# Optimization experiments

Measured on AMD Instinct MI355X. Metric: run time of the kernel, lower is better.

Reference implementation:

```python
import jax, jax.numpy as jnp
import numpy as np

K = 22                       # structuring element is 22x22 ones
ORIGIN = K // 2              # kornia origin = k//2 -> pad (11 before, 10 after)
PAD = ((0, 0), (0, 0), (ORIGIN, K - ORIGIN - 1), (ORIGIN, K - ORIGIN - 1))
WIN = (1, 1, K, K)
STRIDES = (1, 1, 1, 1)


def _erode(x):
    # flat (all-ones) structuring element erosion == sliding-window min.
    # Padding with +inf matches kornia's 'pad with max_val' for erosion.
    return jax.lax.reduce_window(x, float('inf'), jax.lax.min, WIN, STRIDES, PAD)


def _dilate(x):
    # flat dilation == sliding-window max; pad with -inf (kornia pads -max_val).
    return jax.lax.reduce_window(x, float('-inf'), jax.lax.max, WIN, STRIDES, PAD)


def setup_inputs() -> dict:
    key = jax.random.key(0)
    image = jax.random.uniform(key, (8, 3, 1024, 1024), dtype=jnp.float32)
    return {"image": image}


def reference(image):
    # morphological opening = erosion followed by dilation (same kernel)
    return _dilate(_erode(image))
```

## Files before the change

kernel.cpp:

```cpp
#include <hip/hip_runtime.h>


#define HH 1024
#define WW 1024
#define KW 22
#define SB 116
#define PINF __builtin_inff()

template<bool IS_MIN>
__device__ __forceinline__ float vop(float a, float b) {
    return IS_MIN ? fminf(a, b) : fmaxf(a, b);
}

template<bool IS_MIN, int COUT, class Get, class Put>
__device__ __forceinline__ void vanherk(Get get, Put put) {
    constexpr int NIN = COUT + KW - 1;
    constexpr int NB = (NIN + KW - 1) / KW;
    const float ID = IS_MIN ? PINF : -PINF;
    float Sprev[KW];
    #pragma unroll
    for (int j = 0; j < NB; ++j) {
        const int base = KW * j;
        const int needed = (NIN - base) < KW ? (NIN - base) : KW;
        float v[KW];
        #pragma unroll
        for (int m = 0; m < KW; ++m)
            if (m < needed) v[m] = get(base + m);
        float p = ID;
        #pragma unroll
        for (int m = 0; m < KW; ++m) {
            if (m < needed) {
                p = vop<IS_MIN>(p, v[m]);
                const int k = base - (KW - 1) + m;
                if (k >= 0 && k < COUT) {
                    if (m == KW - 1) put(k, p);
                    else             put(k, vop<IS_MIN>(Sprev[m + 1], p));
                }
            }
        }
        if (j < NB - 1) {
            float s = ID;
            #pragma unroll
            for (int m = KW - 1; m >= 0; --m) {
                s = vop<IS_MIN>(s, v[m]);
                Sprev[m] = s;
            }
        }
    }
}

template<bool INTERIOR>
__device__ __forceinline__ void tile_body(const float* __restrict__ src,
                                          float* __restrict__ dst,
                                          int R, int C, float* B, int t) {
    const int w = t >> 6, slot = t & 63;

    if (slot < 54) {
        const int ch = w >> 1;
        const int j = (w & 1) * 54 + slot;
        const int base_o = ch * 43;
        int cj = C - 22 + j;
        bool colOK = true;
        if (!INTERIOR) {
            colOK = (unsigned)cj < WW;
            cj = cj < 0 ? 0 : (cj > WW - 1 ? WW - 1 : cj);
        }
        const float* col = src + cj;
        const int rbase = R - 22 + base_o;
        vanherk<true, 43>(
            [&](int p) {
                int r = rbase + p;
                if (INTERIOR) return col[r * WW];
                int rc = r < 0 ? 0 : (r > HH - 1 ? HH - 1 : r);
                float vv = col[rc * WW];
                return (colOK && (unsigned)r < HH) ? vv : PINF;
            },
            [&](int k, float vv) { B[(base_o + k) * SB + j] = vv; });
    }
    __syncthreads();

    {
        const bool act = t < 255;
        const int ch = (3 * t + 2) >> 8;
        const int o = t - 85 * ch;
        const int g0 = 5 * ch;
        const int c0 = 20 * ch;
        float* Brow = B + o * SB;
        float in12[68];
        if (act) {
            #pragma unroll
            for (int i = 0; i < 17; ++i) {
                float4 x = ((const float4*)Brow)[g0 + i];
                in12[4 * i] = x.x; in12[4 * i + 1] = x.y;
                in12[4 * i + 2] = x.z; in12[4 * i + 3] = x.w;
            }
        }
        float rx[24];
        if (act) {
            float er[45];
            vanherk<true, 45>(
                [&](int p) { return in12[p]; },
                [&](int k, float vv) { er[k] = vv; });
            if (!INTERIOR) {
                const bool rOK = (unsigned)(R - 11 + o) < HH;
                #pragma unroll
                for (int k = 0; k < 45; ++k) {
                    const int cimg = C - 11 + c0 + k;
                    if (!rOK || (unsigned)cimg >= WW) er[k] = -PINF;
                }
            }
            vanherk<false, 24>(
                [&](int p) { return er[p]; },
                [&](int k, float vv) { rx[k] = vv; });
        }
        __syncthreads();
        if (act) {
            #pragma unroll
            for (int i = 0; i < 6; ++i)
                ((float4*)Brow)[g0 + i] =
                    make_float4(rx[4 * i], rx[4 * i + 1],
                                rx[4 * i + 2], rx[4 * i + 3]);
        }
        __syncthreads();
    }

    {
        const int c = t & 63;
        const int y0 = (t >> 6) << 4;
        float o16[16];
        vanherk<false, 16>(
            [&](int p) { return B[(y0 + p) * SB + c]; },
            [&](int k, float vv) { o16[k] = vv; });
        #pragma unroll
        for (int k = 0; k < 16; ++k)
            dst[(R + y0 + k) * WW + C + c] = o16[k];
    }
}

__global__ __launch_bounds__(256, 4) void fused_open(const float* __restrict__ in,
                                                     float* __restrict__ out) {
    __shared__ float B[86 * SB];
    const int t = threadIdx.x;
    const int b = blockIdx.x;
    const int plane = b >> 8;
    const int by = (b >> 4) & 15;
    const int bx = b & 15;
    const int R = by * 64, C = bx * 64;
    const float* src = in + (size_t)plane * (HH * WW);
    float* dst = out + (size_t)plane * (HH * WW);

    if (by >= 1 && by <= 14 && bx >= 1 && bx <= 14)
        tile_body<true>(src, dst, R, C, B, t);
    else
        tile_body<false>(src, dst, R, C, B, t);
}

extern "C" void kernel_launch(void* const* d_in, const int* in_sizes, int n_in,
                              void* d_out, int out_size, void* d_ws, size_t ws_size,
                              hipStream_t stream) {
    const float* in = (const float*)d_in[0];
    float* out = (float*)d_out;
    (void)d_ws; (void)ws_size;
    fused_open<<<24 * 16 * 16, 256, 0, stream>>>(in, out);
}
```

Measured before the change: 184.5 us.

## Reorder separable passes to row-first with vectorized global loads and stores

Changes the fused opening from a column-first order to a row-first order. Each thread now loads a contiguous 68-float row segment with float4 global loads and does the horizontal erosion first. The vertical erosion and dilation then run over shared-memory columns, and a final horizontal dilation writes output with float4 stores. This is meant to replace the strided per-column global reads and scalar stores with coalesced vector accesses, at the cost of a larger shared buffer, more register arrays, and lower lane utilization in some phases.

After: 271.9 us. 47.3% more time.

```diff
diff --git a/kernel.cpp b/kernel.cpp
--- a/kernel.cpp
+++ b/kernel.cpp
@@ -4,7 +4,7 @@
 #define HH 1024
 #define WW 1024
 #define KW 22
-#define SB 116
+#define SB 92
 #define PINF __builtin_inff()
 
 template<bool IS_MIN>
@@ -55,91 +55,114 @@
                                           int R, int C, float* B, int t) {
     const int w = t >> 6, slot = t & 63;
 
-    if (slot < 54) {
-        const int ch = w >> 1;
-        const int j = (w & 1) * 54 + slot;
-        const int base_o = ch * 43;
-        int cj = C - 22 + j;
-        bool colOK = true;
-        if (!INTERIOR) {
-            colOK = (unsigned)cj < WW;
-            cj = cj < 0 ? 0 : (cj > WW - 1 ? WW - 1 : cj);
+    {
+        const bool act = slot < 53;
+        if (act) {
+            const int unit = w * 53 + slot;
+            const int h = unit >= 106;
+            const int i = unit - 106 * h;
+            const int r = R - 22 + i;
+            const int a0 = C - 24 + 44 * h;
+            float in[68];
+            if (INTERIOR) {
+                const float* rowp = src + (size_t)r * WW + a0;
+                #pragma unroll
+                for (int q = 0; q < 17; ++q) {
+                    const float4 x4 = ((const float4*)rowp)[q];
+                    in[4 * q] = x4.x; in[4 * q + 1] = x4.y;
+                    in[4 * q + 2] = x4.z; in[4 * q + 3] = x4.w;
+                }
+            } else {
+                const bool rOK = (unsigned)r < HH;
+                const int rc = r < 0 ? 0 : (r > HH - 1 ? HH - 1 : r);
+                const float* rowp = src + (size_t)rc * WW;
+                #pragma unroll
+                for (int q = 0; q < 68; ++q) {
+                    const int gc = a0 + q;
+                    const bool cOK = (unsigned)gc < WW;
+                    const int gcc = gc < 0 ? 0 : (gc > WW - 1 ? WW - 1 : gc);
+                    const float vv = rowp[gcc];
+                    in[q] = (rOK && cOK) ? vv : PINF;
+                }
+            }
+            float rm[44];
+            vanherk<true, 44>(
+                [&](int p) { return in[2 + p]; },
+                [&](int k, float vv) { rm[k] = vv; });
+            float4* bout = (float4*)(B + i * SB + 44 * h);
+            #pragma unroll
+            for (int q = 0; q < 11; ++q)
+                bout[q] = make_float4(rm[4 * q], rm[4 * q + 1],
+                                      rm[4 * q + 2], rm[4 * q + 3]);
         }
-        const float* col = src + cj;
-        const int rbase = R - 22 + base_o;
-        vanherk<true, 43>(
-            [&](int p) {
-                int r = rbase + p;
-                if (INTERIOR) return col[r * WW];
-                int rc = r < 0 ? 0 : (r > HH - 1 ? HH - 1 : r);
-                float vv = col[rc * WW];
-                return (colOK && (unsigned)r < HH) ? vv : PINF;
-            },
-            [&](int k, float vv) { B[(base_o + k) * SB + j] = vv; });
     }
     __syncthreads();
 
     {
-        const bool act = t < 255;
-        const int ch = (3 * t + 2) >> 8;
-        const int o = t - 85 * ch;
-        const int g0 = 5 * ch;
-        const int c0 = 20 * ch;
-        float* Brow = B + o * SB;
-        float in12[68];
+        const bool act = slot < 43;
+        const int unit = w * 43 + (act ? slot : 0);
+        const int ch = unit >= 86;
+        const int col = unit - 86 * ch;
+        const int base = 32 * ch;
+        float cm[32];
         if (act) {
-            #pragma unroll
-            for (int i = 0; i < 17; ++i) {
-                float4 x = ((const float4*)Brow)[g0 + i];
-                in12[4 * i] = x.x; in12[4 * i + 1] = x.y;
-                in12[4 * i + 2] = x.z; in12[4 * i + 3] = x.w;
-            }
-        }
-        float rx[24];
-        if (act) {
-            float er[45];
-            vanherk<true, 45>(
-                [&](int p) { return in12[p]; },
+            const float* colp = B + col;
+            float er[53];
+            vanherk<true, 53>(
+                [&](int p) { return colp[(base + p) * SB]; },
                 [&](int k, float vv) { er[k] = vv; });
             if (!INTERIOR) {
-                const bool rOK = (unsigned)(R - 11 + o) < HH;
+                const int gc = C - 11 + col;
+                const bool cOK = (unsigned)gc < WW;
                 #pragma unroll
-                for (int k = 0; k < 45; ++k) {
-                    const int cimg = C - 11 + c0 + k;
-                    if (!rOK || (unsigned)cimg >= WW) er[k] = -PINF;
+                for (int k = 0; k < 53; ++k) {
+                    const int ge = R + base - 11 + k;
+                    if (!cOK || (unsigned)ge >= HH) er[k] = -PINF;
                 }
             }
-            vanherk<false, 24>(
+            vanherk<false, 32>(
                 [&](int p) { return er[p]; },
-                [&](int k, float vv) { rx[k] = vv; });
+                [&](int k, float vv) { cm[k] = vv; });
         }
         __syncthreads();
         if (act) {
             #pragma unroll
-            for (int i = 0; i < 6; ++i)
-                ((float4*)Brow)[g0 + i] =
-                    make_float4(rx[4 * i], rx[4 * i + 1],
-                                rx[4 * i + 2], rx[4 * i + 3]);
+            for (int k = 0; k < 32; ++k)
+                B[(base + k) * SB + col] = cm[k];
         }
         __syncthreads();
     }
 
     {
-        const int c = t & 63;
-        const int y0 = (t >> 6) << 4;
-        float o16[16];
-        vanherk<false, 16>(
-            [&](int p) { return B[(y0 + p) * SB + c]; },
-            [&](int k, float vv) { o16[k] = vv; });
-        #pragma unroll
-        for (int k = 0; k < 16; ++k)
-            dst[(R + y0 + k) * WW + C + c] = o16[k];
+        const bool act = slot < 32;
+        if (act) {
+            const int unit = w * 32 + slot;
+            const int y = unit & 63;
+            const int h = unit >> 6;
+            const float* cp = B + y * SB + 32 * h;
+            float in3[56];
+            #pragma unroll
+            for (int q = 0; q < 14; ++q) {
+                const float4 x4 = ((const float4*)cp)[q];
+                in3[4 * q] = x4.x; in3[4 * q + 1] = x4.y;
+                in3[4 * q + 2] = x4.z; in3[4 * q + 3] = x4.w;
+            }
+            float o32[32];
+            vanherk<false, 32>(
+                [&](int p) { return in3[p]; },
+                [&](int k, float vv) { o32[k] = vv; });
+            float4* op = (float4*)(dst + (size_t)(R + y) * WW + C + 32 * h);
+            #pragma unroll
+            for (int q = 0; q < 8; ++q)
+                op[q] = make_float4(o32[4 * q], o32[4 * q + 1],
+                                    o32[4 * q + 2], o32[4 * q + 3]);
+        }
     }
 }
 
 __global__ __launch_bounds__(256, 4) void fused_open(const float* __restrict__ in,
                                                      float* __restrict__ out) {
-    __shared__ float B[86 * SB];
+    __shared__ float B[106 * SB];
     const int t = threadIdx.x;
     const int b = blockIdx.x;
     const int plane = b >> 8;
```
